# Performance work log

Measured on AMD Instinct MI355X. Metric: run time of the kernel, lower is better.

The kernel has to match this reference:

```python
import jax, jax.numpy as jnp
import numpy as np

TOUT = 4096  # fixed padded output frame length (>= max possible cumsum of durations)


def setup_inputs() -> dict:
    key = jax.random.key(0)
    k1, k2 = jax.random.split(key)
    xs = jax.random.normal(k1, (8, 512, 384), dtype=jnp.float32)
    ds = jax.random.randint(k2, (8, 512), 0, 8, dtype=jnp.int64)
    return {"xs": xs, "ds": ds}


def reference(xs, ds):
    # xs: (B, Tin, D) phoneme embeddings; ds: (B, Tin) integer durations.
    # Build mapping matrix M: (B, Tout, Tin) where M[b, t, i] = 1 iff frame t
    # falls in [cumsum(ds)[i] - ds[i], cumsum(ds)[i]), then ys = M @ xs.
    cum = jnp.cumsum(ds, axis=1)          # (B, Tin) right boundaries
    left = cum - ds                        # (B, Tin) left boundaries
    frames = jnp.arange(TOUT)              # (Tout,)
    f = frames[None, :, None]              # (1, Tout, 1)
    M = ((f >= left[:, None, :]) & (f < cum[:, None, :])).astype(xs.dtype)  # (B, Tout, Tin)
    ys = jnp.einsum('bti,bid->btd', M, xs)  # (B, Tout, D)
    return ys
```

## Files before the change

### kernel.cpp

```cpp
#include <hip/hip_runtime.h>

#define NB    8
#define NIN   512
#define TOUT  4096
#define ND    384
#define J4    (ND / 4)
#define TROWS 16
#define BLK   256

typedef float f32x4 __attribute__((ext_vector_type(4)));

__global__ __launch_bounds__(NIN) void build_owner(const int* __restrict__ ds,
                                                   int* __restrict__ owner) {
    const int b   = blockIdx.x;
    const int tid = threadIdx.x;
    __shared__ int wsum[NIN / 64];

    const int d = ds[b * NIN + tid];
    int p = d;
    const int lane = tid & 63;
    const int wid  = tid >> 6;
    #pragma unroll
    for (int off = 1; off < 64; off <<= 1) {
        int v = __shfl_up(p, off, 64);
        if (lane >= off) p += v;
    }
    if (lane == 63) wsum[wid] = p;

    int* ob = owner + b * TOUT;
    #pragma unroll
    for (int t = tid; t < TOUT; t += NIN) ob[t] = -1;
    __syncthreads();

    int acc = 0;
    #pragma unroll
    for (int w = 0; w < NIN / 64; ++w)
        if (w < wid) acc += wsum[w];
    p += acc;
    int right = p < TOUT ? p : TOUT;
    for (int t = p - d; t < right; ++t) ob[t] = tid;
}

__global__ __launch_bounds__(BLK) void gather(const f32x4* __restrict__ xs,
                                              const int* __restrict__ owner,
                                              f32x4* __restrict__ out) {
    const int b       = blockIdx.x & 7;
    const int rowbase = (blockIdx.x >> 3) * TROWS;
    const int tid     = threadIdx.x;

    const int*   ob   = owner + b * TOUT + rowbase;
    const f32x4* xsb  = xs + (size_t)b * NIN * J4;
    f32x4*       outb = out + ((size_t)b * TOUT + rowbase) * J4;

    constexpr int ITER = TROWS * J4 / BLK;
    int   o[ITER];
    f32x4 v[ITER];
    #pragma unroll
    for (int k = 0; k < ITER; ++k)
        o[k] = ob[(k * BLK + tid) / J4];
    #pragma unroll
    for (int k = 0; k < ITER; ++k) {
        const int g = k * BLK + tid;
        const int j = g - (g / J4) * J4;
        v[k] = (f32x4)(0.f);
        if (o[k] >= 0) v[k] = xsb[o[k] * J4 + j];
    }
    #pragma unroll
    for (int k = 0; k < ITER; ++k)
        outb[k * BLK + tid] = v[k];
}

extern "C" void kernel_launch(void* const* d_in, const int* in_sizes, int n_in,
                              void* d_out, int out_size, void* d_ws, size_t ws_size,
                              hipStream_t stream) {
    const float* xs = (const float*)d_in[0];
    const int*   ds = (const int*)d_in[1];
    float* out = (float*)d_out;
    int* owner = (int*)d_ws;

    build_owner<<<NB, NIN, 0, stream>>>(ds, owner);
    gather<<<(TOUT / TROWS) * NB, BLK, 0, stream>>>((const f32x4*)xs, owner,
                                                    (f32x4*)out);
}
```

Before: 76.83 us.

## Fuse owner-map build into gather kernel with per-block prefix scan

Merges the two kernels into one. Each gather block recomputes the duration prefix sum over all 512 tokens and builds its own 32-row owner map in shared memory. This removes the second launch, the global owner buffer round trip, and the dependency between the two kernels. In exchange every block redoes the scan, which is redundant work, and the tile grows to 32 rows with 512 threads.

```diff
diff --git a/kernel.cpp b/kernel.cpp
--- a/kernel.cpp
+++ b/kernel.cpp
@@ -5,16 +5,20 @@
 #define TOUT  4096
 #define ND    384
 #define J4    (ND / 4)
-#define TROWS 16
-#define BLK   256
+#define TROWS 32
+#define BLK   512
 
 typedef float f32x4 __attribute__((ext_vector_type(4)));
 
-__global__ __launch_bounds__(NIN) void build_owner(const int* __restrict__ ds,
-                                                   int* __restrict__ owner) {
-    const int b   = blockIdx.x;
-    const int tid = threadIdx.x;
-    __shared__ int wsum[NIN / 64];
+__global__ __launch_bounds__(BLK) void lenreg(const f32x4* __restrict__ xs,
+                                              const int* __restrict__ ds,
+                                              f32x4* __restrict__ out) {
+    const int b       = blockIdx.x & 7;
+    const int rowbase = (blockIdx.x >> 3) * TROWS;
+    const int tid     = threadIdx.x;
+
+    __shared__ int wsum[BLK / 64];
+    __shared__ int owner[TROWS];
 
     const int d = ds[b * NIN + tid];
     int p = d;
@@ -26,38 +30,31 @@
         if (lane >= off) p += v;
     }
     if (lane == 63) wsum[wid] = p;
+    if (tid < TROWS) owner[tid] = -1;
+    __syncthreads();
+    int acc = 0;
+    #pragma unroll
+    for (int w = 0; w < BLK / 64; ++w)
+        if (w < wid) acc += wsum[w];
+    p += acc;
 
-    int* ob = owner + b * TOUT;
-    #pragma unroll
-    for (int t = tid; t < TOUT; t += NIN) ob[t] = -1;
+    {
+        int lo = p - d;
+        if (lo < rowbase) lo = rowbase;
+        int hi = p;
+        if (hi > rowbase + TROWS) hi = rowbase + TROWS;
+        for (int t = lo; t < hi; ++t) owner[t - rowbase] = tid;
+    }
     __syncthreads();
 
-    int acc = 0;
-    #pragma unroll
-    for (int w = 0; w < NIN / 64; ++w)
-        if (w < wid) acc += wsum[w];
-    p += acc;
-    int right = p < TOUT ? p : TOUT;
-    for (int t = p - d; t < right; ++t) ob[t] = tid;
-}
-
-__global__ __launch_bounds__(BLK) void gather(const f32x4* __restrict__ xs,
-                                              const int* __restrict__ owner,
-                                              f32x4* __restrict__ out) {
-    const int b       = blockIdx.x & 7;
-    const int rowbase = (blockIdx.x >> 3) * TROWS;
-    const int tid     = threadIdx.x;
-
-    const int*   ob   = owner + b * TOUT + rowbase;
     const f32x4* xsb  = xs + (size_t)b * NIN * J4;
     f32x4*       outb = out + ((size_t)b * TOUT + rowbase) * J4;
-
     constexpr int ITER = TROWS * J4 / BLK;
     int   o[ITER];
     f32x4 v[ITER];
     #pragma unroll
     for (int k = 0; k < ITER; ++k)
-        o[k] = ob[(k * BLK + tid) / J4];
+        o[k] = owner[(k * BLK + tid) / J4];
     #pragma unroll
     for (int k = 0; k < ITER; ++k) {
         const int g = k * BLK + tid;
@@ -76,9 +73,7 @@
     const float* xs = (const float*)d_in[0];
     const int*   ds = (const int*)d_in[1];
     float* out = (float*)d_out;
-    int* owner = (int*)d_ws;
 
-    build_owner<<<NB, NIN, 0, stream>>>(ds, owner);
-    gather<<<(TOUT / TROWS) * NB, BLK, 0, stream>>>((const f32x4*)xs, owner,
+    lenreg<<<(TOUT / TROWS) * NB, BLK, 0, stream>>>((const f32x4*)xs, ds,
                                                     (f32x4*)out);
 }
```

After: 77.84 us. No clear change (+1.3%).
